# Performance work log

Measured on AMD Instinct MI355X. Metric: run time of the kernel, lower is better.

The kernel has to match this reference:

```python
import jax, jax.numpy as jnp
import numpy as np

NUM_MODULES = 4
EXPERTS_PER_MODULE = 4
TOTAL_EXPERTS = NUM_MODULES * EXPERTS_PER_MODULE
TOP_K = 4
NORM_TOPK_PROB = True
T = 32768
D = 1536


def setup_inputs() -> dict:
    key = jax.random.key(0)
    k1, k2, k3 = jax.random.split(key, 3)
    hidden_states = jax.random.normal(k1, (T, D), dtype=jnp.float32)
    # nn.Linear weights: (out_features, in_features)
    Wm = jax.random.normal(k2, (NUM_MODULES, D), dtype=jnp.float32) * 0.02
    We = jax.random.normal(k3, (TOTAL_EXPERTS, D), dtype=jnp.float32) * 0.02
    return {"hidden_states": hidden_states, "Wm": Wm, "We": We}


def reference(hidden_states, Wm, We):
    Tn = hidden_states.shape[0]
    # Stage 1: module routing
    module_logits = jnp.einsum('td,md->tm', hidden_states, Wm)  # (T, num_modules)
    module_probs = jax.nn.softmax(module_logits.astype(jnp.float32), axis=-1)
    # Stage 2: expert routing, grouped per module (intra-module softmax)
    expert_logits = jnp.einsum('td,ed->te', hidden_states, We)  # (T, total_experts)
    expert_logits = expert_logits.reshape(Tn, NUM_MODULES, EXPERTS_PER_MODULE)
    expert_probs = jax.nn.softmax(expert_logits.astype(jnp.float32), axis=-1)
    # Combined hierarchical distribution
    combined_probs = (module_probs[:, :, None] * expert_probs).reshape(Tn, TOTAL_EXPERTS)
    # Top-k over flat combined distribution
    top_k_weights, top_k_indices = jax.lax.top_k(combined_probs, TOP_K)
    if NORM_TOPK_PROB:
        top_k_weights = top_k_weights / (jnp.sum(top_k_weights, axis=-1, keepdims=True) + 1e-8)
    top_k_weights = top_k_weights.astype(hidden_states.dtype)
    return combined_probs, top_k_weights, top_k_indices
```

## Files before the change

### kernel.cpp

```cpp
#include <hip/hip_runtime.h>
#include <math.h>


#define DD 1536
#define NM 4
#define NE 16
#define NW 20
#define RPB 128
#define NTHR 512
#define NJ 24
#define WLDS_F (NJ * NW * 64)

typedef float v4f __attribute__((ext_vector_type(4)));

__global__ __launch_bounds__(NTHR)
void router_kernel(const float* __restrict__ hs,
                   const float* __restrict__ Wm,
                   const float* __restrict__ We,
                   float* __restrict__ out,
                   int T)
{
    __shared__ __align__(16) float wl[WLDS_F];
    const int tid  = threadIdx.x;
    const int wv   = tid >> 6;
    const int lane = tid & 63;
    const int q    = lane & 15;
    const int g    = lane >> 4;
    const int rowBlock = blockIdx.x * RPB;

#pragma unroll
    for (int i = 0; i < 15; i++) {
        const int off  = tid * 4 + i * 2048;
        const int j    = off / 1280;
        const int rem  = off - j * 1280;
        const int e    = rem >> 6;
        const int qcol = rem & 63;
        const int col  = j * 64 + qcol;
        v4f w = (e < NE) ? *(const v4f*)(We + (size_t)e * DD + col)
                         : *(const v4f*)(Wm + (size_t)(e - NE) * DD + col);
        *(v4f*)&wl[off] = w;
    }
    __syncthreads();

#pragma unroll 1
    for (int p = 0; p < 2; p++) {
        const int rA = rowBlock + p * 64 + wv * 8 + g;
        const float* hsA = hs + (size_t)rA * DD + q * 4;
        const float* hsB = hsA + 4 * DD;

        float accA[NW], accB[NW];
#pragma unroll
        for (int e = 0; e < NW; e++) { accA[e] = 0.f; accB[e] = 0.f; }

        v4f a0 = *(const v4f*)(hsA);
        v4f b0 = *(const v4f*)(hsB);
        v4f a1 = *(const v4f*)(hsA + 64);
        v4f b1 = *(const v4f*)(hsB + 64);

#pragma unroll 1
        for (int j = 0; j < NJ; j += 2) {
            v4f a2, b2, a3, b3;
            if (j + 2 < NJ) {
                a2 = *(const v4f*)(hsA + (size_t)(j + 2) * 64);
                b2 = *(const v4f*)(hsB + (size_t)(j + 2) * 64);
                a3 = *(const v4f*)(hsA + (size_t)(j + 3) * 64);
                b3 = *(const v4f*)(hsB + (size_t)(j + 3) * 64);
            }
            {
                const float* wb = &wl[j * 1280 + q * 4];
#pragma unroll
                for (int e = 0; e < NW; e++) {
                    v4f w = *(const v4f*)(wb + e * 64);
                    accA[e] = fmaf(a0.x, w.x, accA[e]);
                    accA[e] = fmaf(a0.y, w.y, accA[e]);
                    accA[e] = fmaf(a0.z, w.z, accA[e]);
                    accA[e] = fmaf(a0.w, w.w, accA[e]);
                    accB[e] = fmaf(b0.x, w.x, accB[e]);
                    accB[e] = fmaf(b0.y, w.y, accB[e]);
                    accB[e] = fmaf(b0.z, w.z, accB[e]);
                    accB[e] = fmaf(b0.w, w.w, accB[e]);
                }
            }
            {
                const float* wb = &wl[(j + 1) * 1280 + q * 4];
#pragma unroll
                for (int e = 0; e < NW; e++) {
                    v4f w = *(const v4f*)(wb + e * 64);
                    accA[e] = fmaf(a1.x, w.x, accA[e]);
                    accA[e] = fmaf(a1.y, w.y, accA[e]);
                    accA[e] = fmaf(a1.z, w.z, accA[e]);
                    accA[e] = fmaf(a1.w, w.w, accA[e]);
                    accB[e] = fmaf(b1.x, w.x, accB[e]);
                    accB[e] = fmaf(b1.y, w.y, accB[e]);
                    accB[e] = fmaf(b1.z, w.z, accB[e]);
                    accB[e] = fmaf(b1.w, w.w, accB[e]);
                }
            }
            a0 = a2; b0 = b2; a1 = a3; b1 = b3;
        }

#pragma unroll
        for (int e = 0; e < NW; e++) {
            accA[e] += __shfl_xor(accA[e], 1);
            accA[e] += __shfl_xor(accA[e], 2);
            accA[e] += __shfl_xor(accA[e], 4);
            accA[e] += __shfl_xor(accA[e], 8);
            accB[e] += __shfl_xor(accB[e], 1);
            accB[e] += __shfl_xor(accB[e], 2);
            accB[e] += __shfl_xor(accB[e], 4);
            accB[e] += __shfl_xor(accB[e], 8);
        }

        if (q < 2) {
            float logit[NW];
#pragma unroll
            for (int e = 0; e < NW; e++) logit[e] = q ? accB[e] : accA[e];
            const int row = rA + (q ? 4 : 0);

            float mmax = logit[16];
#pragma unroll
            for (int m = 1; m < NM; m++) mmax = fmaxf(mmax, logit[16 + m]);
            float mexp[NM], msum = 0.f;
#pragma unroll
            for (int m = 0; m < NM; m++) { mexp[m] = expf(logit[16 + m] - mmax); msum += mexp[m]; }

            float comb[NE];
#pragma unroll
            for (int m = 0; m < NM; m++) {
                float mprob = mexp[m] / msum;
                float emax = logit[m * 4];
#pragma unroll
                for (int jj = 1; jj < 4; jj++) emax = fmaxf(emax, logit[m * 4 + jj]);
                float ee[4], esum = 0.f;
#pragma unroll
                for (int jj = 0; jj < 4; jj++) { ee[jj] = expf(logit[m * 4 + jj] - emax); esum += ee[jj]; }
                float scale = mprob / esum;
#pragma unroll
                for (int jj = 0; jj < 4; jj++) comb[m * 4 + jj] = ee[jj] * scale;
            }

            float4* cw = (float4*)(out + (size_t)row * 16);
            cw[0] = make_float4(comb[0],  comb[1],  comb[2],  comb[3]);
            cw[1] = make_float4(comb[4],  comb[5],  comb[6],  comb[7]);
            cw[2] = make_float4(comb[8],  comb[9],  comb[10], comb[11]);
            cw[3] = make_float4(comb[12], comb[13], comb[14], comb[15]);

            float tv[4]; int ti[4];
            unsigned mask = 0;
#pragma unroll
            for (int k = 0; k < 4; k++) {
                float best = -1.f; int bi = 0;
#pragma unroll
                for (int i = 0; i < NE; i++) {
                    bool avail = !((mask >> i) & 1u);
                    if (avail && comb[i] > best) { best = comb[i]; bi = i; }
                }
                tv[k] = best; ti[k] = bi; mask |= 1u << bi;
            }
            float s = tv[0] + tv[1] + tv[2] + tv[3] + 1e-8f;

            const size_t wOff = (size_t)T * 16;
            const size_t iOff = (size_t)T * 20;
            float4* ww = (float4*)(out + wOff + (size_t)row * 4);
            *ww = make_float4(tv[0] / s, tv[1] / s, tv[2] / s, tv[3] / s);
            float4* iw = (float4*)(out + iOff + (size_t)row * 4);
            *iw = make_float4((float)ti[0], (float)ti[1], (float)ti[2], (float)ti[3]);
        }
    }
}

extern "C" void kernel_launch(void* const* d_in, const int* in_sizes, int n_in,
                              void* d_out, int out_size, void* d_ws, size_t ws_size,
                              hipStream_t stream)
{
    const float* hs = (const float*)d_in[0];
    const float* Wm = (const float*)d_in[1];
    const float* We = (const float*)d_in[2];
    float* out = (float*)d_out;
    const int T = in_sizes[0] / DD;
    router_kernel<<<T / RPB, NTHR, 0, stream>>>(hs, Wm, We, out, T);
}
```

Baseline: 292.2 us.

## Stream weights in stages and double-buffer hidden states via direct global-to-LDS loads

The kernel no longer holds all 24 weight chunks in LDS (about 120KB). Weights are now loaded in three stages of 8 chunks, and hidden-state chunks go straight into per-wave LDS double buffers through global_load_lds with manual vmcnt waits. Each block now covers 64 rows instead of 128, and launch bounds ask for 4 blocks per CU. The smaller LDS footprint should let more waves stay resident and hide the memory latency of the bandwidth-bound hidden-state stream. The cost is two extra barriers per stage, weights being reloaded twice as often across blocks, and reliance on hand-written s_waitcnt ordering.

```diff
diff --git a/kernel.cpp b/kernel.cpp
--- a/kernel.cpp
+++ b/kernel.cpp
@@ -6,36 +6,58 @@
 #define NM 4
 #define NE 16
 #define NW 20
-#define RPB 128
 #define NTHR 512
+#define NWAVE 8
+#define RPB 64
 #define NJ 24
-#define WLDS_F (NJ * NW * 64)
+#define SJ 8
+#define NSTAGE 3
+#define WL_F (SJ * NW * 64)
+#define HSB_F (NWAVE * 2 * 512)
 
 typedef float v4f __attribute__((ext_vector_type(4)));
 
-__global__ __launch_bounds__(NTHR)
+__global__ __launch_bounds__(NTHR, 4)
 void router_kernel(const float* __restrict__ hs,
                    const float* __restrict__ Wm,
                    const float* __restrict__ We,
                    float* __restrict__ out,
                    int T)
 {
-    __shared__ __align__(16) float wl[WLDS_F];
+    __shared__ __align__(16) float wl[WL_F];
+    __shared__ __align__(16) float hsb[HSB_F];
     const int tid  = threadIdx.x;
     const int wv   = tid >> 6;
     const int lane = tid & 63;
     const int q    = lane & 15;
     const int g    = lane >> 4;
-    const int rowBlock = blockIdx.x * RPB;
+    const int rW   = blockIdx.x * RPB + wv * 8;
+
+    const float* dmaBase = hs + (size_t)(rW + g) * DD + q * 4;
+    const int hsbOff = __builtin_amdgcn_readfirstlane(wv * 1024);
+
+    float accA[NW], accB[NW];
+#pragma unroll
+    for (int e = 0; e < NW; e++) { accA[e] = 0.f; accB[e] = 0.f; }
+
+    {
+        float* d0 = &hsb[hsbOff];
+        __builtin_amdgcn_global_load_lds(
+            (const __attribute__((address_space(1))) void*)(dmaBase),
+            (__attribute__((address_space(3))) void*)d0, 16, 0, 0);
+        __builtin_amdgcn_global_load_lds(
+            (const __attribute__((address_space(1))) void*)(dmaBase + 4 * DD),
+            (__attribute__((address_space(3))) void*)(d0 + 256), 16, 0, 0);
+    }
 
 #pragma unroll
-    for (int i = 0; i < 15; i++) {
-        const int off  = tid * 4 + i * 2048;
-        const int j    = off / 1280;
-        const int rem  = off - j * 1280;
-        const int e    = rem >> 6;
-        const int qcol = rem & 63;
-        const int col  = j * 64 + qcol;
+    for (int it = 0; it < 5; it++) {
+        const int off = tid * 4 + it * 2048;
+        const int jw  = off / 1280;
+        const int rem = off - jw * 1280;
+        const int e   = rem >> 6;
+        const int qc  = rem & 63;
+        const int col = jw * 64 + qc;
         v4f w = (e < NE) ? *(const v4f*)(We + (size_t)e * DD + col)
                          : *(const v4f*)(Wm + (size_t)(e - NE) * DD + col);
         *(v4f*)&wl[off] = w;
@@ -43,129 +65,116 @@
     __syncthreads();
 
 #pragma unroll 1
-    for (int p = 0; p < 2; p++) {
-        const int rA = rowBlock + p * 64 + wv * 8 + g;
-        const float* hsA = hs + (size_t)rA * DD + q * 4;
-        const float* hsB = hsA + 4 * DD;
+    for (int s = 0; s < NSTAGE; s++) {
+        if (s) {
+            __syncthreads();
+#pragma unroll
+            for (int it = 0; it < 5; it++) {
+                const int off = tid * 4 + it * 2048;
+                const int jw  = off / 1280;
+                const int rem = off - jw * 1280;
+                const int e   = rem >> 6;
+                const int qc  = rem & 63;
+                const int col = (s * SJ + jw) * 64 + qc;
+                v4f w = (e < NE) ? *(const v4f*)(We + (size_t)e * DD + col)
+                                 : *(const v4f*)(Wm + (size_t)(e - NE) * DD + col);
+                *(v4f*)&wl[off] = w;
+            }
+            __syncthreads();
+        }
+#pragma unroll
+        for (int jj = 0; jj < SJ; jj++) {
+            const int j   = s * SJ + jj;
+            const int cur = j & 1;
+            if (j + 1 < NJ) {
+                float* dn = &hsb[hsbOff + (cur ^ 1) * 512];
+                const float* sn = dmaBase + (j + 1) * 64;
+                __builtin_amdgcn_global_load_lds(
+                    (const __attribute__((address_space(1))) void*)sn,
+                    (__attribute__((address_space(3))) void*)dn, 16, 0, 0);
+                __builtin_amdgcn_global_load_lds(
+                    (const __attribute__((address_space(1))) void*)(sn + 4 * DD),
+                    (__attribute__((address_space(3))) void*)(dn + 256), 16, 0, 0);
+                asm volatile("s_waitcnt vmcnt(2)" ::: "memory");
+            } else {
+                asm volatile("s_waitcnt vmcnt(0)" ::: "memory");
+            }
+            v4f h0 = *(const v4f*)&hsb[hsbOff + cur * 512 + g * 64 + q * 4];
+            v4f h1 = *(const v4f*)&hsb[hsbOff + cur * 512 + 256 + g * 64 + q * 4];
+            const float* wb = &wl[jj * 1280 + q * 4];
+#pragma unroll
+            for (int e = 0; e < NW; e++) {
+                v4f w = *(const v4f*)(wb + e * 64);
+                accA[e] = fmaf(h0.x, w.x, accA[e]); accA[e] = fmaf(h0.y, w.y, accA[e]);
+                accA[e] = fmaf(h0.z, w.z, accA[e]); accA[e] = fmaf(h0.w, w.w, accA[e]);
+                accB[e] = fmaf(h1.x, w.x, accB[e]); accB[e] = fmaf(h1.y, w.y, accB[e]);
+                accB[e] = fmaf(h1.z, w.z, accB[e]); accB[e] = fmaf(h1.w, w.w, accB[e]);
+            }
+        }
+    }
 
-        float accA[NW], accB[NW];
 #pragma unroll
-        for (int e = 0; e < NW; e++) { accA[e] = 0.f; accB[e] = 0.f; }
+    for (int e = 0; e < NW; e++) {
+        accA[e] += __shfl_xor(accA[e], 1); accA[e] += __shfl_xor(accA[e], 2);
+        accA[e] += __shfl_xor(accA[e], 4); accA[e] += __shfl_xor(accA[e], 8);
+        accB[e] += __shfl_xor(accB[e], 1); accB[e] += __shfl_xor(accB[e], 2);
+        accB[e] += __shfl_xor(accB[e], 4); accB[e] += __shfl_xor(accB[e], 8);
+    }
 
-        v4f a0 = *(const v4f*)(hsA);
-        v4f b0 = *(const v4f*)(hsB);
-        v4f a1 = *(const v4f*)(hsA + 64);
-        v4f b1 = *(const v4f*)(hsB + 64);
+    if (q < 2) {
+        float logit[NW];
+#pragma unroll
+        for (int e = 0; e < NW; e++) logit[e] = q ? accB[e] : accA[e];
+        const int row = rW + g + (q ? 4 : 0);
 
-#pragma unroll 1
-        for (int j = 0; j < NJ; j += 2) {
-            v4f a2, b2, a3, b3;
-            if (j + 2 < NJ) {
-                a2 = *(const v4f*)(hsA + (size_t)(j + 2) * 64);
-                b2 = *(const v4f*)(hsB + (size_t)(j + 2) * 64);
-                a3 = *(const v4f*)(hsA + (size_t)(j + 3) * 64);
-                b3 = *(const v4f*)(hsB + (size_t)(j + 3) * 64);
-            }
-            {
-                const float* wb = &wl[j * 1280 + q * 4];
+        float mmax = logit[16];
 #pragma unroll
-                for (int e = 0; e < NW; e++) {
-                    v4f w = *(const v4f*)(wb + e * 64);
-                    accA[e] = fmaf(a0.x, w.x, accA[e]);
-                    accA[e] = fmaf(a0.y, w.y, accA[e]);
-                    accA[e] = fmaf(a0.z, w.z, accA[e]);
-                    accA[e] = fmaf(a0.w, w.w, accA[e]);
-                    accB[e] = fmaf(b0.x, w.x, accB[e]);
-                    accB[e] = fmaf(b0.y, w.y, accB[e]);
-                    accB[e] = fmaf(b0.z, w.z, accB[e]);
-                    accB[e] = fmaf(b0.w, w.w, accB[e]);
-                }
-            }
-            {
-                const float* wb = &wl[(j + 1) * 1280 + q * 4];
+        for (int m = 1; m < NM; m++) mmax = fmaxf(mmax, logit[16 + m]);
+        float mexp[NM], msum = 0.f;
 #pragma unroll
-                for (int e = 0; e < NW; e++) {
-                    v4f w = *(const v4f*)(wb + e * 64);
-                    accA[e] = fmaf(a1.x, w.x, accA[e]);
-                    accA[e] = fmaf(a1.y, w.y, accA[e]);
-                    accA[e] = fmaf(a1.z, w.z, accA[e]);
-                    accA[e] = fmaf(a1.w, w.w, accA[e]);
-                    accB[e] = fmaf(b1.x, w.x, accB[e]);
-                    accB[e] = fmaf(b1.y, w.y, accB[e]);
-                    accB[e] = fmaf(b1.z, w.z, accB[e]);
-                    accB[e] = fmaf(b1.w, w.w, accB[e]);
-                }
-            }
-            a0 = a2; b0 = b2; a1 = a3; b1 = b3;
+        for (int m = 0; m < NM; m++) { mexp[m] = expf(logit[16 + m] - mmax); msum += mexp[m]; }
+
+        float comb[NE];
+#pragma unroll
+        for (int m = 0; m < NM; m++) {
+            float mprob = mexp[m] / msum;
+            float emax = logit[m * 4];
+#pragma unroll
+            for (int jj = 1; jj < 4; jj++) emax = fmaxf(emax, logit[m * 4 + jj]);
+            float ee[4], esum = 0.f;
+#pragma unroll
+            for (int jj = 0; jj < 4; jj++) { ee[jj] = expf(logit[m * 4 + jj] - emax); esum += ee[jj]; }
+            float scale = mprob / esum;
+#pragma unroll
+            for (int jj = 0; jj < 4; jj++) comb[m * 4 + jj] = ee[jj] * scale;
         }
 
+        float4* cw = (float4*)(out + (size_t)row * 16);
+        cw[0] = make_float4(comb[0],  comb[1],  comb[2],  comb[3]);
+        cw[1] = make_float4(comb[4],  comb[5],  comb[6],  comb[7]);
+        cw[2] = make_float4(comb[8],  comb[9],  comb[10], comb[11]);
+        cw[3] = make_float4(comb[12], comb[13], comb[14], comb[15]);
+
+        float tv[4]; int ti[4];
+        unsigned mask = 0;
 #pragma unroll
-        for (int e = 0; e < NW; e++) {
-            accA[e] += __shfl_xor(accA[e], 1);
-            accA[e] += __shfl_xor(accA[e], 2);
-            accA[e] += __shfl_xor(accA[e], 4);
-            accA[e] += __shfl_xor(accA[e], 8);
-            accB[e] += __shfl_xor(accB[e], 1);
-            accB[e] += __shfl_xor(accB[e], 2);
-            accB[e] += __shfl_xor(accB[e], 4);
-            accB[e] += __shfl_xor(accB[e], 8);
+        for (int k = 0; k < 4; k++) {
+            float best = -1.f; int bi = 0;
+#pragma unroll
+            for (int i = 0; i < NE; i++) {
+                bool avail = !((mask >> i) & 1u);
+                if (avail && comb[i] > best) { best = comb[i]; bi = i; }
+            }
+            tv[k] = best; ti[k] = bi; mask |= 1u << bi;
         }
+        float s = tv[0] + tv[1] + tv[2] + tv[3] + 1e-8f;
 
-        if (q < 2) {
-            float logit[NW];
-#pragma unroll
-            for (int e = 0; e < NW; e++) logit[e] = q ? accB[e] : accA[e];
-            const int row = rA + (q ? 4 : 0);
-
-            float mmax = logit[16];
-#pragma unroll
-            for (int m = 1; m < NM; m++) mmax = fmaxf(mmax, logit[16 + m]);
-            float mexp[NM], msum = 0.f;
-#pragma unroll
-            for (int m = 0; m < NM; m++) { mexp[m] = expf(logit[16 + m] - mmax); msum += mexp[m]; }
-
-            float comb[NE];
-#pragma unroll
-            for (int m = 0; m < NM; m++) {
-                float mprob = mexp[m] / msum;
-                float emax = logit[m * 4];
-#pragma unroll
-                for (int jj = 1; jj < 4; jj++) emax = fmaxf(emax, logit[m * 4 + jj]);
-                float ee[4], esum = 0.f;
-#pragma unroll
-                for (int jj = 0; jj < 4; jj++) { ee[jj] = expf(logit[m * 4 + jj] - emax); esum += ee[jj]; }
-                float scale = mprob / esum;
-#pragma unroll
-                for (int jj = 0; jj < 4; jj++) comb[m * 4 + jj] = ee[jj] * scale;
-            }
-
-            float4* cw = (float4*)(out + (size_t)row * 16);
-            cw[0] = make_float4(comb[0],  comb[1],  comb[2],  comb[3]);
-            cw[1] = make_float4(comb[4],  comb[5],  comb[6],  comb[7]);
-            cw[2] = make_float4(comb[8],  comb[9],  comb[10], comb[11]);
-            cw[3] = make_float4(comb[12], comb[13], comb[14], comb[15]);
-
-            float tv[4]; int ti[4];
-            unsigned mask = 0;
-#pragma unroll
-            for (int k = 0; k < 4; k++) {
-                float best = -1.f; int bi = 0;
-#pragma unroll
-                for (int i = 0; i < NE; i++) {
-                    bool avail = !((mask >> i) & 1u);
-                    if (avail && comb[i] > best) { best = comb[i]; bi = i; }
-                }
-                tv[k] = best; ti[k] = bi; mask |= 1u << bi;
-            }
-            float s = tv[0] + tv[1] + tv[2] + tv[3] + 1e-8f;
-
-            const size_t wOff = (size_t)T * 16;
-            const size_t iOff = (size_t)T * 20;
-            float4* ww = (float4*)(out + wOff + (size_t)row * 4);
-            *ww = make_float4(tv[0] / s, tv[1] / s, tv[2] / s, tv[3] / s);
-            float4* iw = (float4*)(out + iOff + (size_t)row * 4);
-            *iw = make_float4((float)ti[0], (float)ti[1], (float)ti[2], (float)ti[3]);
-        }
+        const size_t wOff = (size_t)T * 16;
+        const size_t iOff = (size_t)T * 20;
+        float4* ww = (float4*)(out + wOff + (size_t)row * 4);
+        *ww = make_float4(tv[0] / s, tv[1] / s, tv[2] / s, tv[3] / s);
+        float4* iw = (float4*)(out + iOff + (size_t)row * 4);
+        *iw = make_float4((float)ti[0], (float)ti[1], (float)ti[2], (float)ti[3]);
     }
 }
 
```

Measured after the change: 1.008 ms. 245% more time.
